# Kernel tuning notes

Hardware: AMD Instinct MI355X
Metric: run time of the kernel (lower is better)

Reference implementation:

```python
import jax, jax.numpy as jnp
import numpy as np

T, B, E, H, F = 1024, 2, 1024, 16, 8
D = E // H
R = 2 * T - 1  # relative positions T-1 .. -(T-1)


def setup_inputs() -> dict:
    key = jax.random.key(0)
    ks = jax.random.split(key, 11)
    std = float(np.sqrt(2.0 / (E + E)))
    return {
        "input": jax.random.normal(ks[0], (T, B, E), jnp.float32),
        "pos": jax.random.normal(ks[1], (R, B, E), jnp.float32),
        "factor": jax.random.normal(ks[2], (F,), jnp.float32),
        "in_proj_weight": jax.random.normal(ks[3], (3 * E * E, F), jnp.float32) * std,
        "pos_proj_weight": jax.random.normal(ks[4], (E * E, F), jnp.float32) * std,
        "out_proj_weight": jax.random.normal(ks[5], (E * E, F), jnp.float32) * std,
        "in_proj_bias": jax.random.normal(ks[6], (3 * E, F), jnp.float32) * 0.02,
        "pos_proj_bias": jax.random.normal(ks[7], (E, F), jnp.float32) * 0.02,
        "out_proj_bias": jax.random.normal(ks[8], (E, F), jnp.float32) * 0.02,
        "r_w_bias": jax.random.normal(ks[9], (E, F), jnp.float32) * 0.02,
        "r_r_bias": jax.random.normal(ks[10], (E, F), jnp.float32) * 0.02,
    }


def _rel_shift(x):
    # x: [BH, T, R] -> out[b, i, j] = x[b, i, j + (T-1) - i]
    bh, q, r = x.shape
    zp = jnp.zeros((bh, q, 1), x.dtype)
    xp = jnp.concatenate([zp, x], axis=2).reshape(bh, r + 1, q)
    return xp[:, 1:, :].reshape(bh, q, r)


def reference(input, pos, factor, in_proj_weight, pos_proj_weight, out_proj_weight,
              in_proj_bias, pos_proj_bias, out_proj_bias, r_w_bias, r_r_bias):
    # hypernetwork: generate effective weights from factor vector (torch.mv)
    W_in = (in_proj_weight @ factor).reshape(3 * E, E)
    W_pos = (pos_proj_weight @ factor).reshape(E, E)
    W_out = (out_proj_weight @ factor).reshape(E, E)
    b_in = in_proj_bias @ factor
    b_pos = pos_proj_bias @ factor
    b_out = out_proj_bias @ factor
    rw = (r_w_bias @ factor).reshape(H, D)  # content bias
    rr = (r_r_bias @ factor).reshape(H, D)  # position bias

    qkv = input @ W_in.T + b_in                      # [T, B, 3E]
    q, k, v = jnp.split(qkv, 3, axis=-1)
    q = q.reshape(T, B, H, D)
    k = k.reshape(T, B, H, D)
    v = v.reshape(T, B, H, D)
    r = (pos @ W_pos.T + b_pos).reshape(R, B, H, D)  # [R, B, H, D]

    scale = 1.0 / np.sqrt(D)
    # AC: content-content + content bias term
    AC = jnp.einsum('ibhd,jbhd->bhij', q + rw, k)    # [B, H, T, T]
    # BD: content-position + position bias term, then relative shift
    BD = jnp.einsum('ibhd,rbhd->bhir', q + rr, r)    # [B, H, T, R]
    BD = _rel_shift(BD.reshape(B * H, T, R))[:, :, :T].reshape(B, H, T, T)

    attn = jax.nn.softmax((AC + BD) * scale, axis=-1)  # [B, H, T, T]
    out = jnp.einsum('bhij,jbhd->ibhd', attn, v).reshape(T, B, E)
    out = out @ W_out.T + b_out                       # [T, B, E]
    return out
```

## Files before the change

### kernel.cpp

```cpp
#include <hip/hip_runtime.h>


typedef _Float16 h16;
typedef _Float16 h16x8 __attribute__((ext_vector_type(8)));
typedef _Float16 h16x4 __attribute__((ext_vector_type(4)));
typedef float f32x4 __attribute__((ext_vector_type(4)));
typedef uint4 v4u;

static __device__ __forceinline__ f32x4 mfma16(h16x8 a, h16x8 b, f32x4 c) {
  return __builtin_amdgcn_mfma_f32_16x16x32_f16(a, b, c, 0, 0, 0);
}

__global__ __launch_bounds__(256) void hypernet_kernel(
    const float* __restrict__ fac,
    const float* __restrict__ w_in, const float* __restrict__ w_pos,
    const float* __restrict__ w_out, const float* __restrict__ b_in_w,
    const float* __restrict__ b_pos_w, const float* __restrict__ b_out_w,
    const float* __restrict__ rw_w, const float* __restrict__ rr_w,
    h16* __restrict__ Win, h16* __restrict__ Wpos, h16* __restrict__ Wout,
    float* __restrict__ bin, float* __restrict__ bpos, float* __restrict__ bout,
    float* __restrict__ rw, float* __restrict__ rr)
{
  int idx = blockIdx.x * 256 + threadIdx.x;
  float f0=fac[0],f1=fac[1],f2=fac[2],f3=fac[3],f4=fac[4],f5=fac[5],f6=fac[6],f7=fac[7];
#define DOT8(p) ((p)[0]*f0+(p)[1]*f1+(p)[2]*f2+(p)[3]*f3+(p)[4]*f4+(p)[5]*f5+(p)[6]*f6+(p)[7]*f7)
  if (idx < 3145728) { const float* p = w_in  + (size_t)idx*8; Win[idx]  = (h16)DOT8(p); return; }
  idx -= 3145728;
  if (idx < 1048576) { const float* p = w_pos + (size_t)idx*8; Wpos[idx] = (h16)DOT8(p); return; }
  idx -= 1048576;
  if (idx < 1048576) { const float* p = w_out + (size_t)idx*8; Wout[idx] = (h16)DOT8(p); return; }
  idx -= 1048576;
  if (idx < 3072) { bin[idx]  = DOT8(b_in_w  + (size_t)idx*8); return; }
  idx -= 3072;
  if (idx < 1024) { bpos[idx] = DOT8(b_pos_w + (size_t)idx*8); return; }
  idx -= 1024;
  if (idx < 1024) { bout[idx] = DOT8(b_out_w + (size_t)idx*8); return; }
  idx -= 1024;
  if (idx < 1024) { rw[idx]   = DOT8(rw_w    + (size_t)idx*8); return; }
  idx -= 1024;
  if (idx < 1024) { rr[idx]   = DOT8(rr_w    + (size_t)idx*8); return; }
#undef DOT8
}

__global__ __launch_bounds__(256) void cvt_f2h_kernel(
    const float* __restrict__ in, h16* __restrict__ out, int n4)
{
  int i = blockIdx.x * 256 + threadIdx.x;
  if (i >= n4) return;
  float4 v = reinterpret_cast<const float4*>(in)[i];
  h16x4 o = { (h16)v.x, (h16)v.y, (h16)v.z, (h16)v.w };
  reinterpret_cast<h16x4*>(out)[i] = o;
}

__global__ __launch_bounds__(256) void gemm_bt_kernel(
    const h16* __restrict__ A, const h16* __restrict__ Bw,
    const float* __restrict__ bias, float* __restrict__ C,
    int M, int N, int K)
{
  __shared__ __align__(16) h16 a_sm[128*72];
  __shared__ __align__(16) h16 b_sm[128*72];
  const int tid = threadIdx.x, lane = tid & 63, wave = tid >> 6;
  const int quad = lane >> 4, t16 = lane & 15;
  const int wm = wave >> 1, wn = wave & 1;
  const int m0 = blockIdx.y * 128, n0 = blockIdx.x * 128;
  const int srow = tid >> 2, scol = (tid & 3) * 16;

  f32x4 acc[4][4];
#pragma unroll
  for (int i = 0; i < 4; ++i)
#pragma unroll
    for (int j = 0; j < 4; ++j) acc[i][j] = (f32x4){0.f,0.f,0.f,0.f};

  for (int k0 = 0; k0 < K; k0 += 64) {
    __syncthreads();
#pragma unroll
    for (int p = 0; p < 2; ++p) {
      int r = srow + p*64;
      int gm = m0 + r;
      v4u z0 = {0,0,0,0}, z1 = {0,0,0,0};
      if (gm < M) {
        const v4u* s = reinterpret_cast<const v4u*>(A + (size_t)gm*K + k0 + scol);
        z0 = s[0]; z1 = s[1];
      }
      v4u* da = reinterpret_cast<v4u*>(a_sm + r*72 + scol);
      da[0] = z0; da[1] = z1;
      const v4u* sb = reinterpret_cast<const v4u*>(Bw + (size_t)(n0 + r)*K + k0 + scol);
      v4u w0 = sb[0], w1 = sb[1];
      v4u* db = reinterpret_cast<v4u*>(b_sm + r*72 + scol);
      db[0] = w0; db[1] = w1;
    }
    __syncthreads();
#pragma unroll
    for (int kc = 0; kc < 2; ++kc) {
      h16x8 af[4], bfr[4];
#pragma unroll
      for (int i = 0; i < 4; ++i) {
        af[i]  = *reinterpret_cast<const h16x8*>(a_sm + (wm*64 + i*16 + t16)*72 + kc*32 + quad*8);
        bfr[i] = *reinterpret_cast<const h16x8*>(b_sm + (wn*64 + i*16 + t16)*72 + kc*32 + quad*8);
      }
#pragma unroll
      for (int i = 0; i < 4; ++i)
#pragma unroll
        for (int j = 0; j < 4; ++j)
          acc[i][j] = mfma16(af[i], bfr[j], acc[i][j]);
    }
  }
#pragma unroll
  for (int i = 0; i < 4; ++i) {
    int mb = m0 + wm*64 + i*16 + quad*4;
#pragma unroll
    for (int j = 0; j < 4; ++j) {
      int n = n0 + wn*64 + j*16 + t16;
      float bv = bias[n];
#pragma unroll
      for (int r = 0; r < 4; ++r) {
        int m = mb + r;
        if (m < M) C[(size_t)m*N + n] = acc[i][j][r] + bv;
      }
    }
  }
}

__global__ __launch_bounds__(256) void split_cvt_kernel(
    const float* __restrict__ qkv, const float* __restrict__ rproj,
    const float* __restrict__ rw, const float* __restrict__ rr,
    h16* __restrict__ qrw, h16* __restrict__ qrr,
    h16* __restrict__ kb, h16* __restrict__ vb, h16* __restrict__ rb)
{
  int idx = blockIdx.x * 256 + threadIdx.x;
  const int NQ = 32*1024*64;
  if (idx < 4*NQ) {
    int sec = idx >> 21;
    int id  = idx & (NQ - 1);
    int d = id & 63, t = (id >> 6) & 1023, bh = id >> 16;
    int b = bh >> 4, h = bh & 15;
    size_t qoff = (size_t)(t*2 + b) * 3072 + h*64 + d;
    if      (sec == 0) qrw[id] = (h16)(qkv[qoff] + rw[h*64+d]);
    else if (sec == 1) qrr[id] = (h16)(qkv[qoff] + rr[h*64+d]);
    else if (sec == 2) kb[id]  = (h16)qkv[qoff + 1024];
    else               vb[id]  = (h16)qkv[qoff + 2048];
    return;
  }
  idx -= 4*NQ;
  if (idx < 32*2048*64) {
    int d = idx & 63, rel = (idx >> 6) & 2047, bh = idx >> 17;
    int b = bh >> 4, h = bh & 15;
    h16 v = (h16)0.f;
    if (rel < 2047) v = (h16)rproj[(size_t)(rel*2 + b) * 1024 + h*64 + d];
    rb[idx] = v;
  }
}

__global__ __launch_bounds__(256) void flash_kernel(
    const h16* __restrict__ qrw, const h16* __restrict__ qrr,
    const h16* __restrict__ kb, const h16* __restrict__ vb,
    const h16* __restrict__ rb, h16* __restrict__ attn_out)
{
  __shared__ __align__(16) h16 k_sm[64*72];
  __shared__ __align__(16) h16 r_sm[128*72];
  __shared__ __align__(16) h16 vt_sm[64*72];
  __shared__ __align__(16) float bd_sm[4*16*84];

  const int tid = threadIdx.x, lane = tid & 63, wave = tid >> 6;
  const int quad = lane >> 4, t16 = lane & 15;
  const int bh = blockIdx.y;
  const int i0 = blockIdx.x * 64;
  const size_t base  = (size_t)bh * 1024 * 64;
  const size_t rbase = (size_t)bh * 2048 * 64;
  const int iw = i0 + wave * 16;

  h16x8 a_rw[2], a_rr[2];
  {
    const h16* p = qrw + base + (size_t)(iw + t16) * 64 + quad * 8;
    a_rw[0] = *reinterpret_cast<const h16x8*>(p);
    a_rw[1] = *reinterpret_cast<const h16x8*>(p + 32);
    const h16* p2 = qrr + base + (size_t)(iw + t16) * 64 + quad * 8;
    a_rr[0] = *reinterpret_cast<const h16x8*>(p2);
    a_rr[1] = *reinterpret_cast<const h16x8*>(p2 + 32);
  }

  f32x4 o_acc[4];
#pragma unroll
  for (int dc = 0; dc < 4; ++dc) o_acc[dc] = (f32x4){0.f,0.f,0.f,0.f};
  float m_run[4] = {-1e30f,-1e30f,-1e30f,-1e30f};
  float l_run[4] = {0.f,0.f,0.f,0.f};

  float* bdw = bd_sm + wave * (16*84);
  h16*   pw  = reinterpret_cast<h16*>(bdw);

  const int srow = tid >> 2, scol = (tid & 3) * 16;
  const int cb0 = 3 - wave;

  for (int j0 = 0; j0 < 1024; j0 += 64) {
    __syncthreads();
    {
      const v4u* s = reinterpret_cast<const v4u*>(kb + base + (size_t)(j0 + srow)*64 + scol);
      v4u* dst = reinterpret_cast<v4u*>(k_sm + srow*72 + scol);
      dst[0] = s[0]; dst[1] = s[1];
    }
    {
      union { v4u u4[2]; h16 h[16]; } tv;
      const v4u* s = reinterpret_cast<const v4u*>(vb + base + (size_t)(j0 + srow)*64 + scol);
      tv.u4[0] = s[0]; tv.u4[1] = s[1];
#pragma unroll
      for (int e = 0; e < 16; ++e) vt_sm[(scol + e)*72 + srow] = tv.h[e];
    }
    {
      const int rel0 = j0 - i0 + 960;
#pragma unroll
      for (int p = 0; p < 2; ++p) {
        int rrow = srow + p*64;
        const v4u* s = reinterpret_cast<const v4u*>(rb + rbase + (size_t)(rel0 + rrow)*64 + scol);
        v4u* dst = reinterpret_cast<v4u*>(r_sm + rrow*72 + scol);
        dst[0] = s[0]; dst[1] = s[1];
      }
    }
    __syncthreads();

    f32x4 s_ac[4];
#pragma unroll
    for (int c = 0; c < 4; ++c) {
      s_ac[c] = (f32x4){0.f,0.f,0.f,0.f};
#pragma unroll
      for (int kc = 0; kc < 2; ++kc) {
        h16x8 b = *reinterpret_cast<const h16x8*>(k_sm + (c*16 + t16)*72 + kc*32 + quad*8);
        s_ac[c] = mfma16(a_rw[kc], b, s_ac[c]);
      }
    }
    f32x4 s_bd[5];
#pragma unroll
    for (int u = 0; u < 5; ++u) {
      s_bd[u] = (f32x4){0.f,0.f,0.f,0.f};
#pragma unroll
      for (int kc = 0; kc < 2; ++kc) {
        h16x8 b = *reinterpret_cast<const h16x8*>(r_sm + ((cb0+u)*16 + t16)*72 + kc*32 + quad*8);
        s_bd[u] = mfma16(a_rr[kc], b, s_bd[u]);
      }
    }
#pragma unroll
    for (int u = 0; u < 5; ++u)
#pragma unroll
      for (int r = 0; r < 4; ++r)
        bdw[(quad*4 + r)*84 + u*16 + t16] = s_bd[u][r];

    float sv[4][4];
#pragma unroll
    for (int c = 0; c < 4; ++c)
#pragma unroll
      for (int r = 0; r < 4; ++r) {
        int il = quad*4 + r;
        float bdv = bdw[il*84 + c*16 + t16 + 15 - il];
        sv[c][r] = (s_ac[c][r] + bdv) * 0.125f;
      }

    float alpha[4];
#pragma unroll
    for (int r = 0; r < 4; ++r) {
      float v = fmaxf(fmaxf(sv[0][r], sv[1][r]), fmaxf(sv[2][r], sv[3][r]));
#pragma unroll
      for (int off = 1; off < 16; off <<= 1) v = fmaxf(v, __shfl_xor(v, off, 64));
      float mn = fmaxf(m_run[r], v);
      alpha[r] = __expf(m_run[r] - mn);
      m_run[r] = mn;
    }
#pragma unroll
    for (int r = 0; r < 4; ++r) {
      float s0 = 0.f;
#pragma unroll
      for (int c = 0; c < 4; ++c) {
        float p = __expf(sv[c][r] - m_run[r]);
        sv[c][r] = p; s0 += p;
      }
#pragma unroll
      for (int off = 1; off < 16; off <<= 1) s0 += __shfl_xor(s0, off, 64);
      l_run[r] = l_run[r]*alpha[r] + s0;
    }
#pragma unroll
    for (int dc = 0; dc < 4; ++dc) {
      f32x4 t = o_acc[dc];
#pragma unroll
      for (int r = 0; r < 4; ++r) t[r] *= alpha[r];
      o_acc[dc] = t;
    }
#pragma unroll
    for (int c = 0; c < 4; ++c)
#pragma unroll
      for (int r = 0; r < 4; ++r)
        pw[(quad*4 + r)*72 + c*16 + t16] = (h16)sv[c][r];

    h16x8 ap0 = *reinterpret_cast<const h16x8*>(pw + t16*72 + quad*8);
    h16x8 ap1 = *reinterpret_cast<const h16x8*>(pw + t16*72 + 32 + quad*8);
#pragma unroll
    for (int dc = 0; dc < 4; ++dc) {
      h16x8 bv0 = *reinterpret_cast<const h16x8*>(vt_sm + (dc*16 + t16)*72 + quad*8);
      h16x8 bv1 = *reinterpret_cast<const h16x8*>(vt_sm + (dc*16 + t16)*72 + 32 + quad*8);
      o_acc[dc] = mfma16(ap0, bv0, o_acc[dc]);
      o_acc[dc] = mfma16(ap1, bv1, o_acc[dc]);
    }
  }

  const int b = bh >> 4, h = bh & 15;
#pragma unroll
  for (int r = 0; r < 4; ++r) {
    int i = iw + quad*4 + r;
    float inv = 1.f / l_run[r];
#pragma unroll
    for (int dc = 0; dc < 4; ++dc)
      attn_out[(size_t)(i*2 + b)*1024 + h*64 + dc*16 + t16] = (h16)(o_acc[dc][r] * inv);
  }
}

extern "C" void kernel_launch(void* const* d_in, const int* in_sizes, int n_in,
                              void* d_out, int out_size, void* d_ws, size_t ws_size,
                              hipStream_t stream)
{
  const float* input  = (const float*)d_in[0];
  const float* pos    = (const float*)d_in[1];
  const float* fac    = (const float*)d_in[2];
  const float* w_in   = (const float*)d_in[3];
  const float* w_pos  = (const float*)d_in[4];
  const float* w_out  = (const float*)d_in[5];
  const float* bin_w  = (const float*)d_in[6];
  const float* bpos_w = (const float*)d_in[7];
  const float* bout_w = (const float*)d_in[8];
  const float* rw_w   = (const float*)d_in[9];
  const float* rr_w   = (const float*)d_in[10];
  float* out = (float*)d_out;
  (void)in_sizes; (void)n_in; (void)out_size; (void)ws_size;

  char* w = (char*)d_ws;
  auto take = [&](size_t bytes) { char* p = w; w += bytes; return p; };
  h16*   Win    = (h16*)take(3145728ull*2);
  h16*   Wpos   = (h16*)take(1048576ull*2);
  h16*   Wout   = (h16*)take(1048576ull*2);
  float* bin    = (float*)take(3072*4);
  float* bpos   = (float*)take(1024*4);
  float* bout   = (float*)take(1024*4);
  float* rw     = (float*)take(1024*4);
  float* rr     = (float*)take(1024*4);
  h16*   in_h   = (h16*)take(2097152ull*2);
  h16*   pos_h  = (h16*)take(4192256ull*2);
  float* qkv    = (float*)take(6291456ull*4);
  float* rproj  = (float*)take(4192256ull*4);
  h16*   qrwb   = (h16*)take(2097152ull*2);
  h16*   qrrb   = (h16*)take(2097152ull*2);
  h16*   kb     = (h16*)take(2097152ull*2);
  h16*   vb     = (h16*)take(2097152ull*2);
  h16*   rb     = (h16*)take(4194304ull*2);
  h16*   attn_h = (h16*)take(2097152ull*2);

  hypernet_kernel<<<20508, 256, 0, stream>>>(fac, w_in, w_pos, w_out, bin_w, bpos_w, bout_w,
                                             rw_w, rr_w, Win, Wpos, Wout, bin, bpos, bout, rw, rr);
  cvt_f2h_kernel<<<2048, 256, 0, stream>>>(input, in_h, 524288);
  cvt_f2h_kernel<<<4094, 256, 0, stream>>>(pos, pos_h, 1048064);
  gemm_bt_kernel<<<dim3(24, 16), 256, 0, stream>>>(in_h, Win, bin, qkv, 2048, 3072, 1024);
  gemm_bt_kernel<<<dim3(8, 32), 256, 0, stream>>>(pos_h, Wpos, bpos, rproj, 4094, 1024, 1024);
  split_cvt_kernel<<<49152, 256, 0, stream>>>(qkv, rproj, rw, rr, qrwb, qrrb, kb, vb, rb);
  flash_kernel<<<dim3(16, 32), 256, 0, stream>>>(qrwb, qrrb, kb, vb, rb, attn_h);
  gemm_bt_kernel<<<dim3(8, 16), 256, 0, stream>>>(attn_h, Wout, bout, out, 2048, 1024, 1024);
}
```

Baseline: 393.9 us.

## Fuse split/convert into GEMM epilogues, use direct-to-LDS loads, split flash over keys

```diff
diff --git a/kernel.cpp b/kernel.cpp
--- a/kernel.cpp
+++ b/kernel.cpp
@@ -5,10 +5,14 @@
 typedef _Float16 h16x8 __attribute__((ext_vector_type(8)));
 typedef _Float16 h16x4 __attribute__((ext_vector_type(4)));
 typedef float f32x4 __attribute__((ext_vector_type(4)));
-typedef uint4 v4u;
 
 static __device__ __forceinline__ f32x4 mfma16(h16x8 a, h16x8 b, f32x4 c) {
   return __builtin_amdgcn_mfma_f32_16x16x32_f16(a, b, c, 0, 0, 0);
+}
+
+static __device__ __forceinline__ void gload16(const void* g, void* l) {
+  __builtin_amdgcn_global_load_lds((const __attribute__((address_space(1))) void*)g,
+                                   (__attribute__((address_space(3))) void*)l, 16, 0, 0);
 }
 
 __global__ __launch_bounds__(256) void hypernet_kernel(
@@ -19,7 +23,7 @@
     const float* __restrict__ rw_w, const float* __restrict__ rr_w,
     h16* __restrict__ Win, h16* __restrict__ Wpos, h16* __restrict__ Wout,
     float* __restrict__ bin, float* __restrict__ bpos, float* __restrict__ bout,
-    float* __restrict__ rw, float* __restrict__ rr)
+    float* __restrict__ rw, float* __restrict__ rr, h16* __restrict__ rb)
 {
   int idx = blockIdx.x * 256 + threadIdx.x;
   float f0=fac[0],f1=fac[1],f2=fac[2],f3=fac[3],f4=fac[4],f5=fac[5],f6=fac[6],f7=fac[7];
@@ -39,6 +43,10 @@
   if (idx < 1024) { rw[idx]   = DOT8(rw_w    + (size_t)idx*8); return; }
   idx -= 1024;
   if (idx < 1024) { rr[idx]   = DOT8(rr_w    + (size_t)idx*8); return; }
+  idx -= 1024;
+  if (idx < 2048) {
+    rb[(((size_t)(idx >> 6)) << 17) + 2047*64 + (idx & 63)] = (h16)0.f;
+  }
 #undef DOT8
 }
 
@@ -52,18 +60,22 @@
   reinterpret_cast<h16x4*>(out)[i] = o;
 }
 
-__global__ __launch_bounds__(256) void gemm_bt_kernel(
+template <int MODE>
+__global__ __launch_bounds__(256) void gemm_lds_kernel(
     const h16* __restrict__ A, const h16* __restrict__ Bw,
-    const float* __restrict__ bias, float* __restrict__ C,
-    int M, int N, int K)
-{
-  __shared__ __align__(16) h16 a_sm[128*72];
-  __shared__ __align__(16) h16 b_sm[128*72];
+    const float* __restrict__ bias, int M, int N, int K,
+    float* __restrict__ Cout,
+    const float* __restrict__ rwv, const float* __restrict__ rrv,
+    h16* __restrict__ o0, h16* __restrict__ o1,
+    h16* __restrict__ o2, h16* __restrict__ o3)
+{
+  __shared__ __align__(16) h16 a_sm[128*64];
+  __shared__ __align__(16) h16 b_sm[128*64];
   const int tid = threadIdx.x, lane = tid & 63, wave = tid >> 6;
   const int quad = lane >> 4, t16 = lane & 15;
   const int wm = wave >> 1, wn = wave & 1;
   const int m0 = blockIdx.y * 128, n0 = blockIdx.x * 128;
-  const int srow = tid >> 2, scol = (tid & 3) * 16;
+  const int lrow = lane >> 3, lcol = (lane & 7) * 8;
 
   f32x4 acc[4][4];
 #pragma unroll
@@ -74,20 +86,10 @@
   for (int k0 = 0; k0 < K; k0 += 64) {
     __syncthreads();
 #pragma unroll
-    for (int p = 0; p < 2; ++p) {
-      int r = srow + p*64;
-      int gm = m0 + r;
-      v4u z0 = {0,0,0,0}, z1 = {0,0,0,0};
-      if (gm < M) {
-        const v4u* s = reinterpret_cast<const v4u*>(A + (size_t)gm*K + k0 + scol);
-        z0 = s[0]; z1 = s[1];
-      }
-      v4u* da = reinterpret_cast<v4u*>(a_sm + r*72 + scol);
-      da[0] = z0; da[1] = z1;
-      const v4u* sb = reinterpret_cast<const v4u*>(Bw + (size_t)(n0 + r)*K + k0 + scol);
-      v4u w0 = sb[0], w1 = sb[1];
-      v4u* db = reinterpret_cast<v4u*>(b_sm + r*72 + scol);
-      db[0] = w0; db[1] = w1;
+    for (int s = 0; s < 4; ++s) {
+      int rbase = wave*32 + s*8;
+      gload16(A  + (size_t)(m0 + rbase + lrow)*K + k0 + lcol, a_sm + rbase*64);
+      gload16(Bw + (size_t)(n0 + rbase + lrow)*K + k0 + lcol, b_sm + rbase*64);
     }
     __syncthreads();
 #pragma unroll
@@ -95,8 +97,8 @@
       h16x8 af[4], bfr[4];
 #pragma unroll
       for (int i = 0; i < 4; ++i) {
-        af[i]  = *reinterpret_cast<const h16x8*>(a_sm + (wm*64 + i*16 + t16)*72 + kc*32 + quad*8);
-        bfr[i] = *reinterpret_cast<const h16x8*>(b_sm + (wn*64 + i*16 + t16)*72 + kc*32 + quad*8);
+        af[i]  = *reinterpret_cast<const h16x8*>(a_sm + (wm*64 + i*16 + t16)*64 + kc*32 + quad*8);
+        bfr[i] = *reinterpret_cast<const h16x8*>(b_sm + (wn*64 + i*16 + t16)*64 + kc*32 + quad*8);
       }
 #pragma unroll
       for (int i = 0; i < 4; ++i)
@@ -105,6 +107,7 @@
           acc[i][j] = mfma16(af[i], bfr[j], acc[i][j]);
     }
   }
+
 #pragma unroll
   for (int i = 0; i < 4; ++i) {
     int mb = m0 + wm*64 + i*16 + quad*4;
@@ -112,69 +115,82 @@
     for (int j = 0; j < 4; ++j) {
       int n = n0 + wn*64 + j*16 + t16;
       float bv = bias[n];
-#pragma unroll
-      for (int r = 0; r < 4; ++r) {
-        int m = mb + r;
-        if (m < M) C[(size_t)m*N + n] = acc[i][j][r] + bv;
-      }
-    }
-  }
-}
-
-__global__ __launch_bounds__(256) void split_cvt_kernel(
-    const float* __restrict__ qkv, const float* __restrict__ rproj,
-    const float* __restrict__ rw, const float* __restrict__ rr,
-    h16* __restrict__ qrw, h16* __restrict__ qrr,
-    h16* __restrict__ kb, h16* __restrict__ vb, h16* __restrict__ rb)
-{
-  int idx = blockIdx.x * 256 + threadIdx.x;
-  const int NQ = 32*1024*64;
-  if (idx < 4*NQ) {
-    int sec = idx >> 21;
-    int id  = idx & (NQ - 1);
-    int d = id & 63, t = (id >> 6) & 1023, bh = id >> 16;
-    int b = bh >> 4, h = bh & 15;
-    size_t qoff = (size_t)(t*2 + b) * 3072 + h*64 + d;
-    if      (sec == 0) qrw[id] = (h16)(qkv[qoff] + rw[h*64+d]);
-    else if (sec == 1) qrr[id] = (h16)(qkv[qoff] + rr[h*64+d]);
-    else if (sec == 2) kb[id]  = (h16)qkv[qoff + 1024];
-    else               vb[id]  = (h16)qkv[qoff + 2048];
-    return;
-  }
-  idx -= 4*NQ;
-  if (idx < 32*2048*64) {
-    int d = idx & 63, rel = (idx >> 6) & 2047, bh = idx >> 17;
-    int b = bh >> 4, h = bh & 15;
-    h16 v = (h16)0.f;
-    if (rel < 2047) v = (h16)rproj[(size_t)(rel*2 + b) * 1024 + h*64 + d];
-    rb[idx] = v;
-  }
+      if (MODE == 2) {
+#pragma unroll
+        for (int r = 0; r < 4; ++r)
+          Cout[(size_t)(mb + r)*N + n] = acc[i][j][r] + bv;
+      } else if (MODE == 0) {
+        int nn = n & 1023, sec = n >> 10, hh = nn >> 6, d = nn & 63;
+        float rwb = rwv[nn], rrb = rrv[nn];
+#pragma unroll
+        for (int r = 0; r < 4; ++r) {
+          int m = mb + r, t = m >> 1, b = m & 1;
+          size_t off = ((size_t)((b << 4) + hh) << 16) + (t << 6) + d;
+          float v = acc[i][j][r] + bv;
+          if (sec == 0)      { o0[off] = (h16)(v + rwb); o1[off] = (h16)(v + rrb); }
+          else if (sec == 1) { o2[off] = (h16)v; }
+          else               { o3[off] = (h16)v; }
+        }
+      } else {
+        int hh = n >> 6, d = n & 63;
+#pragma unroll
+        for (int r = 0; r < 4; ++r) {
+          int m = mb + r;
+          if (m < M) {
+            int rel = m >> 1, b = m & 1;
+            o0[(((size_t)((b << 4) + hh)) << 17) + (rel << 6) + d] = (h16)(acc[i][j][r] + bv);
+          }
+        }
+      }
+    }
+  }
+}
+
+__global__ __launch_bounds__(256) void transpose_v_kernel(
+    const h16* __restrict__ vb, h16* __restrict__ vbt)
+{
+  __shared__ h16 tile[64*72];
+  const int bh = blockIdx.y, t0 = blockIdx.x * 64;
+  const int r = threadIdx.x >> 3, c = (threadIdx.x & 7) * 8;
+  const h16* src = vb + ((size_t)bh << 16) + (size_t)(t0 + r)*64 + c;
+  *reinterpret_cast<h16x8*>(tile + r*72 + c)        = *reinterpret_cast<const h16x8*>(src);
+  *reinterpret_cast<h16x8*>(tile + (r + 32)*72 + c) = *reinterpret_cast<const h16x8*>(src + 32*64);
+  __syncthreads();
+  h16x8 o0, o1;
+#pragma unroll
+  for (int e = 0; e < 8; ++e) {
+    o0[e] = tile[(c + e)*72 + r];
+    o1[e] = tile[(c + e)*72 + r + 32];
+  }
+  h16* dst = vbt + ((size_t)bh << 16) + (size_t)r*1024 + t0 + c;
+  *reinterpret_cast<h16x8*>(dst)            = o0;
+  *reinterpret_cast<h16x8*>(dst + 32*1024)  = o1;
 }
 
 __global__ __launch_bounds__(256) void flash_kernel(
     const h16* __restrict__ qrw, const h16* __restrict__ qrr,
-    const h16* __restrict__ kb, const h16* __restrict__ vb,
-    const h16* __restrict__ rb, h16* __restrict__ attn_out)
-{
-  __shared__ __align__(16) h16 k_sm[64*72];
-  __shared__ __align__(16) h16 r_sm[128*72];
-  __shared__ __align__(16) h16 vt_sm[64*72];
-  __shared__ __align__(16) float bd_sm[4*16*84];
+    const h16* __restrict__ kb, const h16* __restrict__ vbt,
+    const h16* __restrict__ rb,
+    float* __restrict__ o_part, float* __restrict__ ml_part)
+{
+  __shared__ __align__(16) h16 k_sm[64*64];
+  __shared__ __align__(16) h16 vt_sm[64*64];
+  __shared__ __align__(16) h16 r_sm[128*64];
 
   const int tid = threadIdx.x, lane = tid & 63, wave = tid >> 6;
   const int quad = lane >> 4, t16 = lane & 15;
-  const int bh = blockIdx.y;
-  const int i0 = blockIdx.x * 64;
-  const size_t base  = (size_t)bh * 1024 * 64;
-  const size_t rbase = (size_t)bh * 2048 * 64;
+  const int bh = blockIdx.y, i0 = blockIdx.x * 64, jh = blockIdx.z;
+  const size_t base  = (size_t)bh << 16;
+  const size_t rbase = (size_t)bh << 17;
   const int iw = i0 + wave * 16;
+  const int lrow = lane >> 3, lcol = (lane & 7) * 8;
 
   h16x8 a_rw[2], a_rr[2];
   {
-    const h16* p = qrw + base + (size_t)(iw + t16) * 64 + quad * 8;
+    const h16* p = qrw + base + (size_t)(iw + t16)*64 + quad*8;
     a_rw[0] = *reinterpret_cast<const h16x8*>(p);
     a_rw[1] = *reinterpret_cast<const h16x8*>(p + 32);
-    const h16* p2 = qrr + base + (size_t)(iw + t16) * 64 + quad * 8;
+    const h16* p2 = qrr + base + (size_t)(iw + t16)*64 + quad*8;
     a_rr[0] = *reinterpret_cast<const h16x8*>(p2);
     a_rr[1] = *reinterpret_cast<const h16x8*>(p2 + 32);
   }
@@ -185,34 +201,23 @@
   float m_run[4] = {-1e30f,-1e30f,-1e30f,-1e30f};
   float l_run[4] = {0.f,0.f,0.f,0.f};
 
-  float* bdw = bd_sm + wave * (16*84);
-  h16*   pw  = reinterpret_cast<h16*>(bdw);
-
-  const int srow = tid >> 2, scol = (tid & 3) * 16;
+  h16* bdw = r_sm + wave * (16*84);
   const int cb0 = 3 - wave;
 
-  for (int j0 = 0; j0 < 1024; j0 += 64) {
+  for (int j0 = jh*512; j0 < jh*512 + 512; j0 += 64) {
     __syncthreads();
     {
-      const v4u* s = reinterpret_cast<const v4u*>(kb + base + (size_t)(j0 + srow)*64 + scol);
-      v4u* dst = reinterpret_cast<v4u*>(k_sm + srow*72 + scol);
-      dst[0] = s[0]; dst[1] = s[1];
-    }
-    {
-      union { v4u u4[2]; h16 h[16]; } tv;
-      const v4u* s = reinterpret_cast<const v4u*>(vb + base + (size_t)(j0 + srow)*64 + scol);
-      tv.u4[0] = s[0]; tv.u4[1] = s[1];
-#pragma unroll
-      for (int e = 0; e < 16; ++e) vt_sm[(scol + e)*72 + srow] = tv.h[e];
-    }
-    {
+#pragma unroll
+      for (int s = 0; s < 2; ++s) {
+        int row = wave*16 + s*8;
+        gload16(kb  + base + (size_t)(j0 + row + lrow)*64 + lcol, k_sm  + row*64);
+        gload16(vbt + base + (size_t)(row + lrow)*1024 + j0 + lcol, vt_sm + row*64);
+      }
       const int rel0 = j0 - i0 + 960;
 #pragma unroll
-      for (int p = 0; p < 2; ++p) {
-        int rrow = srow + p*64;
-        const v4u* s = reinterpret_cast<const v4u*>(rb + rbase + (size_t)(rel0 + rrow)*64 + scol);
-        v4u* dst = reinterpret_cast<v4u*>(r_sm + rrow*72 + scol);
-        dst[0] = s[0]; dst[1] = s[1];
+      for (int s = 0; s < 4; ++s) {
+        int row = wave*32 + s*8;
+        gload16(rb + rbase + (size_t)(rel0 + row + lrow)*64 + lcol, r_sm + row*64);
       }
     }
     __syncthreads();
@@ -223,7 +228,7 @@
       s_ac[c] = (f32x4){0.f,0.f,0.f,0.f};
 #pragma unroll
       for (int kc = 0; kc < 2; ++kc) {
-        h16x8 b = *reinterpret_cast<const h16x8*>(k_sm + (c*16 + t16)*72 + kc*32 + quad*8);
+        h16x8 b = *reinterpret_cast<const h16x8*>(k_sm + (c*16 + t16)*64 + kc*32 + quad*8);
         s_ac[c] = mfma16(a_rw[kc], b, s_ac[c]);
       }
     }
@@ -233,15 +238,17 @@
       s_bd[u] = (f32x4){0.f,0.f,0.f,0.f};
 #pragma unroll
       for (int kc = 0; kc < 2; ++kc) {
-        h16x8 b = *reinterpret_cast<const h16x8*>(r_sm + ((cb0+u)*16 + t16)*72 + kc*32 + quad*8);
+        h16x8 b = *reinterpret_cast<const h16x8*>(r_sm + ((cb0+u)*16 + t16)*64 + kc*32 + quad*8);
         s_bd[u] = mfma16(a_rr[kc], b, s_bd[u]);
       }
     }
+    __syncthreads();
+
 #pragma unroll
     for (int u = 0; u < 5; ++u)
 #pragma unroll
       for (int r = 0; r < 4; ++r)
-        bdw[(quad*4 + r)*84 + u*16 + t16] = s_bd[u][r];
+        bdw[(quad*4 + r)*84 + u*16 + t16] = (h16)s_bd[u][r];
 
     float sv[4][4];
 #pragma unroll
@@ -249,7 +256,7 @@
 #pragma unroll
       for (int r = 0; r < 4; ++r) {
         int il = quad*4 + r;
-        float bdv = bdw[il*84 + c*16 + t16 + 15 - il];
+        float bdv = (float)bdw[il*84 + c*16 + t16 + 15 - il];
         sv[c][r] = (s_ac[c][r] + bdv) * 0.125f;
       }
 
@@ -282,6 +289,7 @@
       for (int r = 0; r < 4; ++r) t[r] *= alpha[r];
       o_acc[dc] = t;
     }
+    h16* pw = bdw;
 #pragma unroll
     for (int c = 0; c < 4; ++c)
 #pragma unroll
@@ -292,22 +300,46 @@
     h16x8 ap1 = *reinterpret_cast<const h16x8*>(pw + t16*72 + 32 + quad*8);
 #pragma unroll
     for (int dc = 0; dc < 4; ++dc) {
-      h16x8 bv0 = *reinterpret_cast<const h16x8*>(vt_sm + (dc*16 + t16)*72 + quad*8);
-      h16x8 bv1 = *reinterpret_cast<const h16x8*>(vt_sm + (dc*16 + t16)*72 + 32 + quad*8);
+      h16x8 bv0 = *reinterpret_cast<const h16x8*>(vt_sm + (dc*16 + t16)*64 + quad*8);
+      h16x8 bv1 = *reinterpret_cast<const h16x8*>(vt_sm + (dc*16 + t16)*64 + 32 + quad*8);
       o_acc[dc] = mfma16(ap0, bv0, o_acc[dc]);
       o_acc[dc] = mfma16(ap1, bv1, o_acc[dc]);
     }
   }
 
-  const int b = bh >> 4, h = bh & 15;
+  const size_t obase = ((size_t)jh*32 + bh) * 1024 * 64;
 #pragma unroll
   for (int r = 0; r < 4; ++r) {
     int i = iw + quad*4 + r;
-    float inv = 1.f / l_run[r];
 #pragma unroll
     for (int dc = 0; dc < 4; ++dc)
-      attn_out[(size_t)(i*2 + b)*1024 + h*64 + dc*16 + t16] = (h16)(o_acc[dc][r] * inv);
-  }
+      o_part[obase + (size_t)i*64 + dc*16 + t16] = o_acc[dc][r];
+    if (t16 == 0) {
+      size_t mo = (((size_t)jh*32 + bh)*1024 + i)*2;
+      ml_part[mo]     = m_run[r];
+      ml_part[mo + 1] = l_run[r];
+    }
+  }
+}
+
+__global__ __launch_bounds__(256) void combine_kernel(
+    const float* __restrict__ o_part, const float* __restrict__ ml_part,
+    h16* __restrict__ attn_h)
+{
+  int gid = blockIdx.x * 256 + threadIdx.x;
+  int row = gid >> 4;
+  int d4 = (gid & 15) * 4;
+  float m1 = ml_part[row*2], l1 = ml_part[row*2 + 1];
+  float m2 = ml_part[65536 + row*2], l2 = ml_part[65536 + row*2 + 1];
+  float M = fmaxf(m1, m2);
+  float e1 = __expf(m1 - M), e2 = __expf(m2 - M);
+  float inv = 1.f / (e1*l1 + e2*l2);
+  float4 O1 = *reinterpret_cast<const float4*>(o_part + (size_t)row*64 + d4);
+  float4 O2 = *reinterpret_cast<const float4*>(o_part + 2097152 + (size_t)row*64 + d4);
+  int bh = row >> 10, i = row & 1023, b = bh >> 4, h = bh & 15;
+  h16x4 o = { (h16)((e1*O1.x + e2*O2.x) * inv), (h16)((e1*O1.y + e2*O2.y) * inv),
+              (h16)((e1*O1.z + e2*O2.z) * inv), (h16)((e1*O1.w + e2*O2.w) * inv) };
+  *reinterpret_cast<h16x4*>(attn_h + ((size_t)(i*2 + b))*1024 + h*64 + d4) = o;
 }
 
 extern "C" void kernel_launch(void* const* d_in, const int* in_sizes, int n_in,
@@ -340,22 +372,28 @@
   float* rr     = (float*)take(1024*4);
   h16*   in_h   = (h16*)take(2097152ull*2);
   h16*   pos_h  = (h16*)take(4192256ull*2);
-  float* qkv    = (float*)take(6291456ull*4);
-  float* rproj  = (float*)take(4192256ull*4);
   h16*   qrwb   = (h16*)take(2097152ull*2);
   h16*   qrrb   = (h16*)take(2097152ull*2);
   h16*   kb     = (h16*)take(2097152ull*2);
   h16*   vb     = (h16*)take(2097152ull*2);
+  h16*   vbt    = (h16*)take(2097152ull*2);
   h16*   rb     = (h16*)take(4194304ull*2);
+  float* o_part = (float*)take(4194304ull*4);
+  float* ml     = (float*)take(131072ull*4);
   h16*   attn_h = (h16*)take(2097152ull*2);
 
-  hypernet_kernel<<<20508, 256, 0, stream>>>(fac, w_in, w_pos, w_out, bin_w, bpos_w, bout_w,
-                                             rw_w, rr_w, Win, Wpos, Wout, bin, bpos, bout, rw, rr);
+  hypernet_kernel<<<20516, 256, 0, stream>>>(fac, w_in, w_pos, w_out, bin_w, bpos_w, bout_w,
+                                             rw_w, rr_w, Win, Wpos, Wout, bin, bpos, bout,
+                                             rw, rr, rb);
   cvt_f2h_kernel<<<2048, 256, 0, stream>>>(input, in_h, 524288);
   cvt_f2h_kernel<<<4094, 256, 0, stream>>>(pos, pos_h, 1048064);
-  gemm_bt_kernel<<<dim3(24, 16), 256, 0, stream>>>(in_h, Win, bin, qkv, 2048, 3072, 1024);
-  gemm_bt_kernel<<<dim3(8, 32), 256, 0, stream>>>(pos_h, Wpos, bpos, rproj, 4094, 1024, 1024);
-  split_cvt_kernel<<<49152, 256, 0, stream>>>(qkv, rproj, rw, rr, qrwb, qrrb, kb, vb, rb);
-  flash_kernel<<<dim3(16, 32), 256, 0, stream>>>(qrwb, qrrb, kb, vb, rb, attn_h);
-  gemm_bt_kernel<<<dim3(8, 16), 256, 0, stream>>>(attn_h, Wout, bout, out, 2048, 1024, 1024);
-}
+  gemm_lds_kernel<0><<<dim3(24, 16), 256, 0, stream>>>(in_h, Win, bin, 2048, 3072, 1024,
+                                                       nullptr, rw, rr, qrwb, qrrb, kb, vb);
+  gemm_lds_kernel<1><<<dim3(8, 32), 256, 0, stream>>>(pos_h, Wpos, bpos, 4094, 1024, 1024,
+                                                      nullptr, nullptr, nullptr, rb, nullptr, nullptr, nullptr);
+  transpose_v_kernel<<<dim3(16, 32), 256, 0, stream>>>(vb, vbt);
+  flash_kernel<<<dim3(16, 32, 2), 256, 0, stream>>>(qrwb, qrrb, kb, vbt, rb, o_part, ml);
+  combine_kernel<<<2048, 256, 0, stream>>>(o_part, ml, attn_h);
+  gemm_lds_kernel<2><<<dim3(8, 16), 256, 0, stream>>>(attn_h, Wout, bout, 2048, 1024, 1024,
+                                                      out, nullptr, nullptr, nullptr, nullptr, nullptr, nullptr);
+}
```

New measurement: 379.0 us. 3.8% less time.
